# Optimization experiments

Measured on AMD Instinct MI355X. Metric: run time of the kernel, lower is better.

The kernel has to match this reference:

```python
import jax, jax.numpy as jnp
import numpy as np

D_OUT = 32
INPUT_LEN = 2048
NUM_EIGH = 32
K_U = 3
K_Y = 2


def _top_hankel_eigh(n, k):
    # Hankel matrix Z[i,j] = 2 / ((i+j)^3 - (i+j)) for i,j in 1..n
    i = np.arange(1, n + 1, dtype=np.float64)
    s = i[:, None] + i[None, :]
    Z = 2.0 / (s ** 3 - s)
    vals, vecs = np.linalg.eigh(Z)
    return (jnp.asarray(vals[-k:], dtype=jnp.float32),
            jnp.asarray(vecs[:, -k:], dtype=jnp.float32))


def setup_inputs() -> dict:
    key = jax.random.key(0)
    k1, k2, k3, k4 = jax.random.split(key, 4)
    B = 32
    inputs = jax.random.normal(k1, (B, INPUT_LEN, D_OUT), dtype=jnp.float32)
    eig_vals, eig_vecs = _top_hankel_eigh(INPUT_LEN, NUM_EIGH)
    m_u = jax.random.normal(k2, (D_OUT, D_OUT, K_U), dtype=jnp.float32) * 0.02
    m_phi = jax.random.normal(k3, (D_OUT * NUM_EIGH, D_OUT), dtype=jnp.float32) * 0.02
    m_y = jax.random.normal(k4, (D_OUT, K_Y, D_OUT), dtype=jnp.float32) * 0.02
    return {"inputs": inputs, "eig_vals": eig_vals, "eig_vecs": eig_vecs,
            "m_u": m_u, "m_phi": m_phi, "m_y": m_y}


def _spectral_conv(v, u):
    # Causal FFT convolution of each filter v[:,k] with each channel u[:,:,d].
    # v: (l, k), u: (b, l, d) -> (b, l, k, d)
    l = v.shape[0]
    n = 2 * l
    V = jnp.fft.rfft(v, n=n, axis=0)          # (nf, k)
    U = jnp.fft.rfft(u, n=n, axis=1)          # (b, nf, d)
    P = V[None, :, :, None] * U[:, :, None, :]  # (b, nf, k, d)
    return jnp.fft.irfft(P, n=n, axis=1)[:, :l]


def _compute_x_tilde(inputs, eig_vals, eig_vecs):
    b, l, d = inputs.shape
    x_tilde = _spectral_conv(eig_vecs, inputs)                  # (b, l, k, d)
    x_tilde = x_tilde * (eig_vals ** 0.25)[None, None, :, None]
    return x_tilde.reshape(b, l, -1)                            # (b, l, k*d)


def _compute_ar_x_preds(w, x):
    # w: (d_out, d_in, k), x: (b, l, d_in) -> (b, l, d_out)
    d_out, d_in, k = w.shape
    b, l, _ = x.shape
    o = jnp.einsum('oik,bli->bklo', w, x)                       # (b, k, l, d_out)
    shifts = jnp.arange(k)
    rolled = jax.vmap(lambda oi, s: jnp.roll(oi, s, axis=1),
                      in_axes=(1, 0), out_axes=1)(o, shifts)    # (b, k, l, d_out)
    mask = (jnp.arange(l)[None, :] >= shifts[:, None]).astype(x.dtype)  # (k, l)
    return jnp.sum(rolled * mask[None, :, :, None], axis=1)


def _compute_y_t(m_y, deltas):
    # m_y: (d_out, k_y, d_out), deltas: (b, l, d_out)
    # y_t = sum_{j<k_y} m_y[:, j] @ y_{t-1-j} + delta_t
    b, l, d = deltas.shape
    ky = m_y.shape[1]
    carry0 = jnp.zeros((b, ky, d), dtype=deltas.dtype)

    def step(carry, x):
        out = jnp.einsum('oki,bki->bo', m_y, carry) + x
        carry = jnp.roll(carry, 1, axis=1).at[:, 0].set(out)
        return carry, out

    _, ys = jax.lax.scan(step, carry0, jnp.swapaxes(deltas, 0, 1))
    return jnp.swapaxes(ys, 0, 1)


def reference(inputs, eig_vals, eig_vecs, m_u, m_phi, m_y):
    x_tilde = _compute_x_tilde(inputs, eig_vals, eig_vecs)
    delta_phi = x_tilde @ m_phi
    delta_ar_u = _compute_ar_x_preds(m_u, inputs)
    return _compute_y_t(m_y, delta_phi + delta_ar_u)
```

## Files before the change

### kernel.cpp

```cpp
#include <hip/hip_runtime.h>
#include <math.h>

#define L     2048
#define NFFT  4096
#define NH    2049
#define UST   2052
#define D     32
#define B     32
#define KU    3
#define CCH   64
#define NCH   32

__device__ __forceinline__ int PHY(int i) { return i + (i >> 5); }
__device__ __forceinline__ int REV4(int i) {
  int r2 = __brev(i) >> 20;
  return ((r2 & 0x555) << 1) | ((r2 >> 1) & 0x555);
}

__global__ void k_init_tw(float2* __restrict__ tw) {
  int j = blockIdx.x * blockDim.x + threadIdx.x;
  if (j < NFFT) {
    double ang = -2.0 * 3.14159265358979323846 * (double)j / (double)NFFT;
    tw[j] = make_float2((float)cos(ang), (float)sin(ang));
  }
}

__device__ void dif6(float* sre, float* sim, const float2* __restrict__ tw, int tid) {
  #pragma unroll
  for (int st = 0; st < 6; ++st) {
    const int shift = 10 - 2 * st;
    const int q = 1 << shift;
    const int r = 1 << (2 * st);
    #pragma unroll
    for (int h = 0; h < 2; ++h) {
      const int idx = tid + h * 512;
      const int j = idx & (q - 1);
      const int g = idx >> shift;
      const int i0 = (g << (shift + 2)) + j;
      const int p0 = PHY(i0), p1 = PHY(i0 + q), p2 = PHY(i0 + 2 * q), p3 = PHY(i0 + 3 * q);
      float ax = sre[p0], ay = sim[p0], bx = sre[p1], by = sim[p1];
      float cx = sre[p2], cy = sim[p2], dx = sre[p3], dy = sim[p3];
      float t0x = ax + cx, t0y = ay + cy, t1x = ax - cx, t1y = ay - cy;
      float t2x = bx + dx, t2y = by + dy, t3x = bx - dx, t3y = by - dy;
      float2 w1 = tw[j * r];
      float w2x = w1.x * w1.x - w1.y * w1.y, w2y = 2.f * w1.x * w1.y;
      float w3x = w2x * w1.x - w2y * w1.y, w3y = w2x * w1.y + w2y * w1.x;
      sre[p0] = t0x + t2x; sim[p0] = t0y + t2y;
      float u1x = t1x + t3y, u1y = t1y - t3x;
      sre[p1] = u1x * w1.x - u1y * w1.y; sim[p1] = u1x * w1.y + u1y * w1.x;
      float u2x = t0x - t2x, u2y = t0y - t2y;
      sre[p2] = u2x * w2x - u2y * w2y; sim[p2] = u2x * w2y + u2y * w2x;
      float u3x = t1x - t3y, u3y = t1y + t3x;
      sre[p3] = u3x * w3x - u3y * w3y; sim[p3] = u3x * w3y + u3y * w3x;
    }
    __syncthreads();
  }
}

__device__ void dit6(float* sre, float* sim, const float2* __restrict__ tw, int tid) {
  #pragma unroll
  for (int st = 0; st < 6; ++st) {
    const int shift = 2 * st;
    const int q = 1 << shift;
    const int r = 1 << (10 - 2 * st);
    #pragma unroll
    for (int h = 0; h < 2; ++h) {
      const int idx = tid + h * 512;
      const int j = idx & (q - 1);
      const int g = idx >> shift;
      const int i0 = (g << (shift + 2)) + j;
      const int p0 = PHY(i0), p1 = PHY(i0 + q), p2 = PHY(i0 + 2 * q), p3 = PHY(i0 + 3 * q);
      float ax = sre[p0], ay = sim[p0], bx = sre[p1], by = sim[p1];
      float cx = sre[p2], cy = sim[p2], dx = sre[p3], dy = sim[p3];
      float2 w1 = tw[j * r]; w1.y = -w1.y;
      float w2x = w1.x * w1.x - w1.y * w1.y, w2y = 2.f * w1.x * w1.y;
      float w3x = w2x * w1.x - w2y * w1.y, w3y = w2x * w1.y + w2y * w1.x;
      float bpx = bx * w1.x - by * w1.y, bpy = bx * w1.y + by * w1.x;
      float cpx = cx * w2x - cy * w2y,   cpy = cx * w2y + cy * w2x;
      float dpx = dx * w3x - dy * w3y,   dpy = dx * w3y + dy * w3x;
      float t0x = ax + cpx, t0y = ay + cpy, t1x = ax - cpx, t1y = ay - cpy;
      float t2x = bpx + dpx, t2y = bpy + dpy, t3x = bpx - dpx, t3y = bpy - dpy;
      sre[p0] = t0x + t2x; sim[p0] = t0y + t2y;
      sre[p1] = t1x - t3y; sim[p1] = t1y + t3x;
      sre[p2] = t0x - t2x; sim[p2] = t0y - t2y;
      sre[p3] = t1x + t3y; sim[p3] = t1y - t3x;
    }
    __syncthreads();
  }
}

__global__ __launch_bounds__(256) void k_tr(const float* __restrict__ u,
                                            float2* __restrict__ uTp) {
  __shared__ float tile[64][33];
  const int b = blockIdx.y;
  const int t0 = blockIdx.x * 64;
  const int tid = threadIdx.x;
  for (int i = tid; i < 64 * 32; i += 256) {
    int tl = i >> 5, d = i & 31;
    tile[tl][d] = u[((size_t)b * L + t0 + tl) * D + d];
  }
  __syncthreads();
  for (int i = tid; i < 16 * 64; i += 256) {
    int p = i >> 6, tt = i & 63;
    uTp[((size_t)b * 16 + p) * L + t0 + tt] =
        make_float2(tile[tt][2 * p], tile[tt][2 * p + 1]);
  }
}

__global__ __launch_bounds__(512) void k_fft_fwd(const float2* __restrict__ uTp,
                                                 const float* __restrict__ eig_vecs,
                                                 const float* __restrict__ eig_vals,
                                                 const float2* __restrict__ tw,
                                                 float2* __restrict__ Ubuf,
                                                 float2* __restrict__ Vf) {
  __shared__ float sre[4224];
  __shared__ float sim[4224];
  const int blk = blockIdx.x;
  const int tid = threadIdx.x;
  if (blk < 512) {
    const float2* zp = uTp + (size_t)blk * L;
    for (int t = tid; t < L; t += 512) {
      float2 z = zp[t];
      int p = PHY(t);
      sre[p] = z.x; sim[p] = z.y;
    }
  } else {
    const int p2 = blk - 512;
    for (int t = tid; t < L; t += 512) {
      int p = PHY(t);
      sre[p] = eig_vecs[(size_t)t * D + 2 * p2];
      sim[p] = eig_vecs[(size_t)t * D + 2 * p2 + 1];
    }
  }
  for (int t = L + tid; t < NFFT; t += 512) {
    int p = PHY(t);
    sre[p] = 0.f; sim[p] = 0.f;
  }
  __syncthreads();
  dif6(sre, sim, tw, tid);
  if (blk < 512) {
    float2* r0 = Ubuf + (size_t)(2 * blk) * UST;
    float2* r1 = r0 + UST;
    for (int f = tid; f <= 2048; f += 512) {
      int pa = PHY(REV4(f));
      int pc = PHY(REV4((NFFT - f) & (NFFT - 1)));
      float Ax = sre[pa], Ay = sim[pa];
      float Bx = sre[pc], By = -sim[pc];
      r0[f] = make_float2(0.5f * (Ax + Bx), 0.5f * (Ay + By));
      float Dx = Ax - Bx, Dy = Ay - By;
      r1[f] = make_float2(0.5f * Dy, -0.5f * Dx);
    }
  } else {
    const int p2 = blk - 512;
    const float sc0 = powf(eig_vals[2 * p2], 0.25f);
    const float sc1 = powf(eig_vals[2 * p2 + 1], 0.25f);
    float2* r0 = Vf + (size_t)(2 * p2) * UST;
    float2* r1 = r0 + UST;
    for (int f = tid; f <= 2048; f += 512) {
      int pa = PHY(REV4(f));
      int pc = PHY(REV4((NFFT - f) & (NFFT - 1)));
      float Ax = sre[pa], Ay = sim[pa];
      float Bx = sre[pc], By = -sim[pc];
      r0[f] = make_float2(0.5f * sc0 * (Ax + Bx), 0.5f * sc0 * (Ay + By));
      float Dx = Ax - Bx, Dy = Ay - By;
      r1[f] = make_float2(0.5f * sc1 * Dy, -0.5f * sc1 * Dx);
    }
  }
}

__global__ __launch_bounds__(1024) void k_w(const float2* __restrict__ Vf,
                                            const float* __restrict__ m_phi,
                                            float2* __restrict__ Wm) {
  __shared__ float2 vl[D];
  const int f = blockIdx.x, tid = threadIdx.x;
  if (tid < D) vl[tid] = Vf[(size_t)tid * UST + f];
  __syncthreads();
  const int d = tid >> 5, o = tid & 31;
  float2 acc = make_float2(0.f, 0.f);
  #pragma unroll
  for (int k = 0; k < D; ++k) {
    float m = m_phi[(k * D + d) * D + o];
    float2 v = vl[k];
    acc.x += v.x * m;
    acc.y += v.y * m;
  }
  Wm[(size_t)f * D * D + d * D + o] = acc;
}

#define FT 4
__global__ __launch_bounds__(128) void k_mix(const float2* __restrict__ Ubuf,
                                             const float2* __restrict__ Wm,
                                             float2* __restrict__ Qbuf) {
  __shared__ float2 Wl[FT][D * D];
  __shared__ float2 Ul[D][FT];
  const int f0 = blockIdx.x * FT;
  const int tid = threadIdx.x;
  for (int idx = tid; idx < FT * D * D; idx += 128) {
    int fi = idx >> 10, rest = idx & 1023;
    int f = f0 + fi;
    Wl[fi][rest] = (f < NH) ? Wm[(size_t)f * D * D + rest] : make_float2(0.f, 0.f);
  }
  const int fi = tid & (FT - 1);
  const int o  = tid >> 2;
  const int f  = f0 + fi;
  const int ld = tid >> 2, lf = tid & 3;
  for (int b = 0; b < B; ++b) {
    {
      int ff = f0 + lf;
      Ul[ld][lf] = (ff < NH) ? Ubuf[((size_t)b * D + ld) * UST + ff]
                             : make_float2(0.f, 0.f);
    }
    __syncthreads();
    float2 acc = make_float2(0.f, 0.f);
    #pragma unroll
    for (int d2 = 0; d2 < D; ++d2) {
      float2 uu = Ul[d2][fi];
      float2 ww = Wl[fi][d2 * D + o];
      acc.x += uu.x * ww.x - uu.y * ww.y;
      acc.y += uu.x * ww.y + uu.y * ww.x;
    }
    if (f < NH) Qbuf[((size_t)b * D + o) * UST + f] = acc;
    __syncthreads();
  }
}

__global__ __launch_bounds__(512) void k_ifft(const float2* __restrict__ Qbuf,
                                              const float2* __restrict__ tw,
                                              float* __restrict__ dT) {
  __shared__ float sre[4224];
  __shared__ float sim[4224];
  const int blk = blockIdx.x;
  const int tid = threadIdx.x;
  const float2* r0 = Qbuf + (size_t)(2 * blk) * UST;
  const float2* r1 = r0 + UST;
  for (int f = tid; f <= 2048; f += 512) {
    float2 q1 = r0[f], q2 = r1[f];
    int pa = PHY(REV4(f));
    int pc = PHY(REV4((NFFT - f) & (NFFT - 1)));
    sre[pa] = q1.x - q2.y; sim[pa] = q1.y + q2.x;
    sre[pc] = q1.x + q2.y; sim[pc] = -q1.y + q2.x;
  }
  __syncthreads();
  dit6(sre, sim, tw, tid);
  float* d0 = dT + (size_t)(2 * blk) * L;
  float* d1 = d0 + L;
  const float inv = 1.0f / (float)NFFT;
  for (int t = tid; t < L; t += 512) {
    int p = PHY(t);
    d0[t] = sre[p] * inv;
    d1[t] = sim[p] * inv;
  }
}

#define TT 64
__global__ __launch_bounds__(256) void k_ar(const float* __restrict__ dT,
                                            const float* __restrict__ u,
                                            const float* __restrict__ m_u,
                                            float* __restrict__ delta) {
  __shared__ float Ds[D][TT + 1];
  __shared__ float Us[TT + 2][D];
  __shared__ float Mt[KU][D][D];
  const int b = blockIdx.y;
  const int t0 = blockIdx.x * TT;
  const int tid = threadIdx.x;
  for (int idx = tid; idx < D * D * KU; idx += blockDim.x) {
    int k = idx % KU, i = (idx / KU) % D, o = idx / (KU * D);
    Mt[k][i][o] = m_u[idx];
  }
  for (int idx = tid; idx < D * TT; idx += blockDim.x) {
    int o = idx >> 6, tt = idx & 63;
    Ds[o][tt] = dT[((size_t)b * D + o) * L + t0 + tt];
  }
  for (int idx = tid; idx < (TT + 2) * D; idx += blockDim.x) {
    int j = idx >> 5, i = idx & 31;
    int t = t0 - 2 + j;
    Us[j][i] = (t >= 0) ? u[((size_t)b * L + t) * D + i] : 0.f;
  }
  __syncthreads();
  const int o = tid & 31, ts = tid >> 5;
  for (int tt = ts; tt < TT; tt += 8) {
    int t = t0 + tt;
    float acc = Ds[o][tt];
    #pragma unroll
    for (int k2 = 0; k2 < KU; ++k2) {
      if (t >= k2) {
        const float* ur = Us[tt + 2 - k2];
        #pragma unroll
        for (int i = 0; i < D; ++i) acc += Mt[k2][i][o] * ur[i];
      }
    }
    delta[((size_t)b * L + t) * D + o] = acc;
  }
}

__global__ __launch_bounds__(1024) void k_tc(const float* __restrict__ m_y,
                                             float* __restrict__ Tc) {
  __shared__ float A[64][68];
  __shared__ float Bb[64][68];
  const int tid = threadIdx.x;
  for (int idx = tid; idx < 64 * 64; idx += blockDim.x) {
    int r = idx >> 6, c = idx & 63;
    float v;
    if (r < 32) v = m_y[(r * 2 + (c >> 5)) * D + (c & 31)];
    else        v = (c == r - 32) ? 1.f : 0.f;
    A[r][c] = v;
  }
  __syncthreads();
  const int r = tid >> 4, cg = tid & 15;
  for (int it = 0; it < 6; ++it) {
    float4 acc = make_float4(0.f, 0.f, 0.f, 0.f);
    for (int i = 0; i < 64; ++i) {
      float a = A[r][i];
      float4 v = *(const float4*)&A[i][cg * 4];
      acc.x += a * v.x; acc.y += a * v.y; acc.z += a * v.z; acc.w += a * v.w;
    }
    __syncthreads();
    *(float4*)&Bb[r][cg * 4] = acc;
    __syncthreads();
    *(float4*)&A[r][cg * 4] = *(const float4*)&Bb[r][cg * 4];
    __syncthreads();
  }
  for (int idx = tid; idx < 64 * 64; idx += blockDim.x)
    Tc[idx] = A[idx >> 6][idx & 63];
}

__global__ void k_scanA(const float* __restrict__ delta,
                        const float* __restrict__ m_y,
                        float* __restrict__ shat) {
  __shared__ float yb[2][D];
  const int b = blockIdx.y, c = blockIdx.x;
  const int lane = threadIdx.x;
  const int o = lane & 31, h = lane >> 5;
  float m0[16], m1[16];
  #pragma unroll
  for (int i = 0; i < 16; ++i) {
    m0[i] = m_y[(o * 2 + 0) * D + h * 16 + i];
    m1[i] = m_y[(o * 2 + 1) * D + h * 16 + i];
  }
  if (lane < D) { yb[0][lane] = 0.f; yb[1][lane] = 0.f; }
  __syncthreads();
  const float* dp = delta + ((size_t)b * L + c * CCH) * D;
  float ylast = 0.f, yprev = 0.f;
  for (int r = 0; r < CCH; ++r) {
    const float* y1 = yb[(r + 1) & 1];
    const float* y2 = yb[r & 1];
    float acc = 0.f;
    #pragma unroll
    for (int i = 0; i < 16; ++i)
      acc += m0[i] * y1[h * 16 + i] + m1[i] * y2[h * 16 + i];
    acc += __shfl_xor(acc, 32);
    float y = acc + dp[r * D + o];
    __syncthreads();
    if (h == 0) yb[r & 1][o] = y;
    __syncthreads();
    yprev = ylast; ylast = y;
  }
  if (h == 0) {
    float* sp = shat + ((size_t)b * NCH + c) * 64;
    sp[o] = ylast;
    sp[32 + o] = yprev;
  }
}

__global__ void k_scanB(const float* __restrict__ Tc,
                        const float* __restrict__ shat,
                        float* __restrict__ sin_) {
  __shared__ float TcT[64][65];
  __shared__ float sb[64];
  const int b = blockIdx.x;
  const int r = threadIdx.x;
  for (int idx = r; idx < 64 * 64; idx += 64) {
    int rr = idx >> 6, cc = idx & 63;
    TcT[cc][rr] = Tc[idx];
  }
  sb[r] = 0.f;
  __syncthreads();
  for (int c = 0; c < NCH; ++c) {
    sin_[((size_t)b * NCH + c) * 64 + r] = sb[r];
    float acc = 0.f;
    #pragma unroll 8
    for (int i = 0; i < 64; ++i) acc += TcT[i][r] * sb[i];
    acc += shat[((size_t)b * NCH + c) * 64 + r];
    __syncthreads();
    sb[r] = acc;
    __syncthreads();
  }
}

__global__ void k_scanC(const float* __restrict__ delta,
                        const float* __restrict__ m_y,
                        const float* __restrict__ sin_,
                        float* __restrict__ out) {
  __shared__ float yb[2][D];
  const int b = blockIdx.y, c = blockIdx.x;
  const int lane = threadIdx.x;
  const int o = lane & 31, h = lane >> 5;
  float m0[16], m1[16];
  #pragma unroll
  for (int i = 0; i < 16; ++i) {
    m0[i] = m_y[(o * 2 + 0) * D + h * 16 + i];
    m1[i] = m_y[(o * 2 + 1) * D + h * 16 + i];
  }
  const float* sp = sin_ + ((size_t)b * NCH + c) * 64;
  if (lane < 32) yb[1][lane] = sp[lane];
  else           yb[0][lane - 32] = sp[lane];
  __syncthreads();
  const float* dp = delta + ((size_t)b * L + c * CCH) * D;
  float* op = out + ((size_t)b * L + c * CCH) * D;
  for (int r = 0; r < CCH; ++r) {
    const float* y1 = yb[(r + 1) & 1];
    const float* y2 = yb[r & 1];
    float acc = 0.f;
    #pragma unroll
    for (int i = 0; i < 16; ++i)
      acc += m0[i] * y1[h * 16 + i] + m1[i] * y2[h * 16 + i];
    acc += __shfl_xor(acc, 32);
    float y = acc + dp[r * D + o];
    __syncthreads();
    if (h == 0) { yb[r & 1][o] = y; op[r * D + o] = y; }
    __syncthreads();
  }
}

extern "C" void kernel_launch(void* const* d_in, const int* in_sizes, int n_in,
                              void* d_out, int out_size, void* d_ws, size_t ws_size,
                              hipStream_t stream) {
  const float* u        = (const float*)d_in[0];
  const float* eig_vals = (const float*)d_in[1];
  const float* eig_vecs = (const float*)d_in[2];
  const float* m_u      = (const float*)d_in[3];
  const float* m_phi    = (const float*)d_in[4];
  const float* m_y      = (const float*)d_in[5];
  float* out = (float*)d_out;

  char* ws = (char*)d_ws;
  size_t off = 0;
  auto alloc = [&](size_t bytes) -> void* {
    void* p = ws + off;
    off += bytes;
    off = (off + 255) & ~(size_t)255;
    return p;
  };
  float2* tw   = (float2*)alloc((size_t)NFFT * sizeof(float2));
  float2* uTp  = (float2*)alloc((size_t)B * 16 * L * sizeof(float2));
  float2* Vf   = (float2*)alloc((size_t)D * UST * sizeof(float2));
  float2* Wm   = (float2*)alloc((size_t)NH * D * D * sizeof(float2));
  float2* Ubuf = (float2*)alloc((size_t)B * D * UST * sizeof(float2));
  float2* Qbuf = (float2*)alloc((size_t)B * D * UST * sizeof(float2));
  float*  Tc   = (float*)alloc(64 * 64 * sizeof(float));
  float*  shat = (float*)alloc((size_t)B * NCH * 64 * sizeof(float));
  float*  sinb = (float*)alloc((size_t)B * NCH * 64 * sizeof(float));
  float* dT    = (float*)uTp;
  float* delta = (float*)Ubuf;

  k_init_tw<<<16, 256, 0, stream>>>(tw);
  k_tr     <<<dim3(L / 64, B), 256, 0, stream>>>(u, uTp);
  k_fft_fwd<<<528, 512, 0, stream>>>(uTp, eig_vecs, eig_vals, tw, Ubuf, Vf);
  k_w      <<<NH, 1024, 0, stream>>>(Vf, m_phi, Wm);
  k_mix    <<<(NH + FT - 1) / FT, 128, 0, stream>>>(Ubuf, Wm, Qbuf);
  k_ifft   <<<B * 16, 512, 0, stream>>>(Qbuf, tw, dT);
  k_ar     <<<dim3(L / TT, B), 256, 0, stream>>>(dT, u, m_u, delta);
  k_tc     <<<1, 1024, 0, stream>>>(m_y, Tc);
  k_scanA  <<<dim3(NCH, B), 64, 0, stream>>>(delta, m_y, shat);
  k_scanB  <<<B, 64, 0, stream>>>(Tc, shat, sinb);
  k_scanC  <<<dim3(NCH, B), 64, 0, stream>>>(delta, m_y, sinb, out);
}
```

Baseline: 307.0 us.

## Hold mixing weights in registers and batch eight inputs per mix step

The frequency-domain channel-mixing kernel now keeps each thread's weight column in registers instead of staging all weights in shared memory. It processes eight batch elements per synchronization round, with eight frequencies per block and 256 threads. Outputs go through a skewed shared-memory tile so stores to the transposed output are coalesced along frequency. This cuts shared-memory traffic and barrier count, at the cost of more registers per thread (32 float2 for weights) and possibly lower occupancy.

```diff
diff --git a/kernel.cpp b/kernel.cpp
--- a/kernel.cpp
+++ b/kernel.cpp
@@ -187,39 +187,59 @@
   Wm[(size_t)f * D * D + d * D + o] = acc;
 }
 
-#define FT 4
-__global__ __launch_bounds__(128) void k_mix(const float2* __restrict__ Ubuf,
+#define FT 8
+#define BC 8
+__global__ __launch_bounds__(256) void k_mix(const float2* __restrict__ Ubuf,
                                              const float2* __restrict__ Wm,
                                              float2* __restrict__ Qbuf) {
-  __shared__ float2 Wl[FT][D * D];
-  __shared__ float2 Ul[D][FT];
+  __shared__ float2 Ul[BC][D][FT];
+  __shared__ float2 Qs[BC][D][FT];
   const int f0 = blockIdx.x * FT;
   const int tid = threadIdx.x;
-  for (int idx = tid; idx < FT * D * D; idx += 128) {
-    int fi = idx >> 10, rest = idx & 1023;
-    int f = f0 + fi;
-    Wl[fi][rest] = (f < NH) ? Wm[(size_t)f * D * D + rest] : make_float2(0.f, 0.f);
-  }
-  const int fi = tid & (FT - 1);
-  const int o  = tid >> 2;
-  const int f  = f0 + fi;
-  const int ld = tid >> 2, lf = tid & 3;
-  for (int b = 0; b < B; ++b) {
-    {
+  const int o = tid & 31, fi = tid >> 5;
+  const int f = f0 + fi;
+  float2 Wr[D];
+  if (f < NH) {
+    const float2* wp = Wm + (size_t)f * D * D + o;
+    #pragma unroll
+    for (int d = 0; d < D; ++d) Wr[d] = wp[d * D];
+  } else {
+    #pragma unroll
+    for (int d = 0; d < D; ++d) Wr[d] = make_float2(0.f, 0.f);
+  }
+  const int lf = tid & 7, row = tid >> 3;
+  for (int b0 = 0; b0 < B; b0 += BC) {
+    #pragma unroll
+    for (int it = 0; it < 8; ++it) {
+      int r = row + it * 32;
+      int bc = r >> 5, d = r & 31;
       int ff = f0 + lf;
-      Ul[ld][lf] = (ff < NH) ? Ubuf[((size_t)b * D + ld) * UST + ff]
-                             : make_float2(0.f, 0.f);
-    }
-    __syncthreads();
-    float2 acc = make_float2(0.f, 0.f);
-    #pragma unroll
-    for (int d2 = 0; d2 < D; ++d2) {
-      float2 uu = Ul[d2][fi];
-      float2 ww = Wl[fi][d2 * D + o];
-      acc.x += uu.x * ww.x - uu.y * ww.y;
-      acc.y += uu.x * ww.y + uu.y * ww.x;
-    }
-    if (f < NH) Qbuf[((size_t)b * D + o) * UST + f] = acc;
+      Ul[bc][d][lf] = (ff < NH)
+          ? Ubuf[((size_t)(b0 + bc) * D + d) * UST + ff]
+          : make_float2(0.f, 0.f);
+    }
+    __syncthreads();
+    #pragma unroll
+    for (int bc = 0; bc < BC; ++bc) {
+      float ax = 0.f, ay = 0.f;
+      #pragma unroll
+      for (int d = 0; d < D; ++d) {
+        float2 uu = Ul[bc][d][fi];
+        float2 ww = Wr[d];
+        ax += uu.x * ww.x - uu.y * ww.y;
+        ay += uu.x * ww.y + uu.y * ww.x;
+      }
+      Qs[bc][o][(fi + o) & 7] = make_float2(ax, ay);
+    }
+    __syncthreads();
+    #pragma unroll
+    for (int it = 0; it < 8; ++it) {
+      int r = row + it * 32;
+      int bc = r >> 5, oo = r & 31;
+      int ff = f0 + lf;
+      if (ff < NH)
+        Qbuf[((size_t)(b0 + bc) * D + oo) * UST + ff] = Qs[bc][oo][(lf + oo) & 7];
+    }
     __syncthreads();
   }
 }
@@ -457,7 +477,7 @@
   k_tr     <<<dim3(L / 64, B), 256, 0, stream>>>(u, uTp);
   k_fft_fwd<<<528, 512, 0, stream>>>(uTp, eig_vecs, eig_vals, tw, Ubuf, Vf);
   k_w      <<<NH, 1024, 0, stream>>>(Vf, m_phi, Wm);
-  k_mix    <<<(NH + FT - 1) / FT, 128, 0, stream>>>(Ubuf, Wm, Qbuf);
+  k_mix    <<<(NH + FT - 1) / FT, 256, 0, stream>>>(Ubuf, Wm, Qbuf);
   k_ifft   <<<B * 16, 512, 0, stream>>>(Qbuf, tw, dT);
   k_ar     <<<dim3(L / TT, B), 256, 0, stream>>>(dT, u, m_u, delta);
   k_tc     <<<1, 1024, 0, stream>>>(m_y, Tc);
```

After: 278.6 us. 1.1x faster.
